# Optimization experiments

Hardware: AMD Instinct MI355X
Metric: run time of the kernel (lower is better)

## Reference

```python
import jax, jax.numpy as jnp
import numpy as np

LAMBDA_SCALE = 0.5
EPS = 1e-6

def setup_inputs() -> dict:
    key = jax.random.key(0)
    ks = jax.random.split(key, 9)
    B, S, D, E, F = 4, 2048, 1024, 8, 4096
    x = jax.random.normal(ks[0], (B, S, D), dtype=jnp.float32)
    prev_logits = jax.random.normal(ks[1], (B, S, E), dtype=jnp.float32)
    # router params (nn.Linear default init scale ~ 1/sqrt(fan_in))
    Wt = jax.random.normal(ks[2], (E, D), dtype=jnp.float32) / np.sqrt(D)
    Wgt = jax.random.normal(ks[3], (E, E), dtype=jnp.float32) / np.sqrt(E)
    We_logits = jnp.zeros((E,), dtype=jnp.float32)
    # expert MLPs, stacked over the expert axis
    W1 = jax.random.normal(ks[4], (E, D, F), dtype=jnp.float32) / np.sqrt(D)
    b1 = jax.random.normal(ks[5], (E, F), dtype=jnp.float32) * 0.01
    W2 = jax.random.normal(ks[6], (E, F, D), dtype=jnp.float32) / np.sqrt(F)
    b2 = jax.random.normal(ks[7], (E, D), dtype=jnp.float32) * 0.01
    return {"x": x, "prev_logits": prev_logits, "Wt": Wt, "Wgt": Wgt,
            "We_logits": We_logits, "W1": W1, "b1": b1, "W2": W2, "b2": b2}

def reference(x, prev_logits, Wt, Wgt, We_logits, W1, b1, W2, b2):
    # router logits: [B,S,E]
    logits = jnp.einsum('bsd,ed->bse', x, Wt) + jnp.einsum('bse,fe->bsf', prev_logits, Wgt)
    st = jax.nn.softmax(logits, axis=-1)
    We = jax.nn.sigmoid(We_logits)                      # [E]
    mask = (st > LAMBDA_SCALE * We).astype(st.dtype)    # data-dependent gate mask
    g = st * mask                                       # [B,S,E]
    # dense per-expert MLP over all tokens (faithful to the module)
    h = jax.nn.gelu(jnp.einsum('bsd,edf->bsef', x, W1) + b1, approximate=False)  # [B,S,E,F]
    outk = jnp.einsum('bsef,efd->bsed', h, W2) + b2     # [B,S,E,D]
    y = jnp.einsum('bse,bsed->bsd', g, outk)
    y = y / (jnp.sum(g, axis=-1, keepdims=True) + EPS)
    return (y, jax.lax.stop_gradient(logits))
```

## Files before the change

### kernel.cpp

```cpp
#include <hip/hip_runtime.h>
#include <math.h>

#define NTOK 8192
#define DDIM 1024
#define NEXP 8
#define FDIM 4096
#define MAXROWS 25600

typedef short bf16x8 __attribute__((ext_vector_type(8)));
typedef float f32x4 __attribute__((ext_vector_type(4)));

static __device__ __forceinline__ unsigned short f2bf(float f) {
  unsigned int u = __float_as_uint(f);
  u += 0x7fffu + ((u >> 16) & 1u);
  return (unsigned short)(u >> 16);
}

static __device__ __forceinline__ void gl_lds16(const void* g, void* l) {
  __builtin_amdgcn_global_load_lds(
      (const __attribute__((address_space(1))) unsigned int*)g,
      (__attribute__((address_space(3))) unsigned int*)l, 16, 0, 0);
}

__global__ __launch_bounds__(256) void router_kernel(
    const float* __restrict__ x, const float* __restrict__ prev,
    const float* __restrict__ Wt, const float* __restrict__ Wgt,
    const float* __restrict__ Wel,
    float* __restrict__ gn, float* __restrict__ logits_out)
{
  __shared__ float wt_s[NEXP * DDIM];
  const int tid = threadIdx.x;
  for (int i = tid; i < NEXP * DDIM; i += 256) wt_s[i] = Wt[i];
  __syncthreads();
  const int lane = tid & 63;
  const int t = blockIdx.x * 4 + (tid >> 6);

  const float* xr = x + (size_t)t * DDIM;
  float acc[NEXP];
#pragma unroll
  for (int e = 0; e < NEXP; ++e) acc[e] = 0.f;
  for (int k = lane; k < DDIM; k += 64) {
    float xv = xr[k];
#pragma unroll
    for (int e = 0; e < NEXP; ++e) acc[e] += xv * wt_s[e * DDIM + k];
  }
#pragma unroll
  for (int e = 0; e < NEXP; ++e) {
    float v = acc[e];
#pragma unroll
    for (int off = 32; off >= 1; off >>= 1) v += __shfl_xor(v, off);
    acc[e] = v;
  }
  float pl[NEXP];
#pragma unroll
  for (int e = 0; e < NEXP; ++e) pl[e] = prev[(size_t)t * NEXP + e];
#pragma unroll
  for (int e = 0; e < NEXP; ++e) {
    float s = acc[e];
#pragma unroll
    for (int e2 = 0; e2 < NEXP; ++e2) s += pl[e2] * Wgt[e * NEXP + e2];
    acc[e] = s;
  }
  float mx = acc[0];
#pragma unroll
  for (int e = 1; e < NEXP; ++e) mx = fmaxf(mx, acc[e]);
  float st[NEXP]; float se = 0.f;
#pragma unroll
  for (int e = 0; e < NEXP; ++e) { st[e] = expf(acc[e] - mx); se += st[e]; }
  float inv = 1.f / se;
  float g[NEXP]; float gs = 0.f;
#pragma unroll
  for (int e = 0; e < NEXP; ++e) {
    float s = st[e] * inv;
    float we = 1.f / (1.f + expf(-Wel[e]));
    float gg = (s > 0.5f * we) ? s : 0.f;
    g[e] = gg; gs += gg;
  }
  float r = 1.f / (gs + 1e-6f);
  if (lane < NEXP) {
    gn[(size_t)t * NEXP + lane] = g[lane] * r;
    logits_out[(size_t)t * NEXP + lane] = acc[lane];
  }
}

__global__ __launch_bounds__(256) void cast_kernel(
    const float* __restrict__ in, unsigned short* __restrict__ out)
{
  size_t i = ((size_t)blockIdx.x * 256 + threadIdx.x) * 8;
  float4 a = *(const float4*)(in + i);
  float4 b = *(const float4*)(in + i + 4);
  unsigned short tb[8];
  tb[0]=f2bf(a.x); tb[1]=f2bf(a.y); tb[2]=f2bf(a.z); tb[3]=f2bf(a.w);
  tb[4]=f2bf(b.x); tb[5]=f2bf(b.y); tb[6]=f2bf(b.z); tb[7]=f2bf(b.w);
  *(uint4*)(out + i) = *(const uint4*)tb;
}

__global__ __launch_bounds__(256) void count_kernel(
    const float* __restrict__ gn, int* __restrict__ cnt)
{
  const int e = blockIdx.x, tid = threadIdx.x;
  int c = 0;
  for (int t = tid; t < NTOK; t += 256) c += (gn[(size_t)t * NEXP + e] > 0.f) ? 1 : 0;
#pragma unroll
  for (int o = 32; o >= 1; o >>= 1) c += __shfl_xor(c, o);
  __shared__ int sm[4];
  if ((tid & 63) == 0) sm[tid >> 6] = c;
  __syncthreads();
  if (tid == 0) cnt[e] = sm[0] + sm[1] + sm[2] + sm[3];
}

__global__ __launch_bounds__(256) void compact_kernel(
    const float* __restrict__ gn, const int* __restrict__ cnt,
    int* __restrict__ offs, int* __restrict__ rowtok, int* __restrict__ rowof)
{
  const int e = blockIdx.x, tid = threadIdx.x;
  int base = 0;
#pragma unroll
  for (int q = 0; q < 8; ++q) if (q < e) base += (cnt[q] + 127) & ~127;
  const int padcnt = (cnt[e] + 127) & ~127;
  if (e == 0 && tid == 0) {
    int a = 0; offs[0] = 0;
#pragma unroll
    for (int q = 0; q < 8; ++q) { a += (cnt[q] + 127) & ~127; offs[q + 1] = a; }
  }
  __shared__ int wsm[4];
  __shared__ int running;
  if (tid == 0) running = 0;
  __syncthreads();
  const int lane = tid & 63, wv = tid >> 6;
  for (int c0 = 0; c0 < NTOK; c0 += 256) {
    const int t = c0 + tid;
    const bool pr = gn[(size_t)t * NEXP + e] > 0.f;
    unsigned long long bal = __ballot(pr);
    int pre = __popcll(bal & ((1ull << lane) - 1ull));
    if (lane == 0) wsm[wv] = __popcll(bal);
    __syncthreads();
    int wbase = 0;
#pragma unroll
    for (int q = 0; q < 4; ++q) if (q < wv) wbase += wsm[q];
    const int tot = wsm[0] + wsm[1] + wsm[2] + wsm[3];
    const int idx = base + running + wbase + pre;
    if (pr) rowtok[idx] = t;
    rowof[(size_t)t * NEXP + e] = pr ? idx : -1;
    __syncthreads();
    if (tid == 0) running += tot;
  }
  __syncthreads();
  for (int i = cnt[e] + tid; i < padcnt; i += 256) rowtok[base + i] = -1;
}

__global__ __launch_bounds__(256) void y_init_kernel(
    const float* __restrict__ gn, const float* __restrict__ b2,
    float* __restrict__ y)
{
  const int t = blockIdx.y;
  const int d = blockIdx.x * 256 + threadIdx.x;
  float s = 0.f;
#pragma unroll
  for (int e = 0; e < NEXP; ++e) s += gn[(size_t)t * NEXP + e] * b2[(size_t)e * DDIM + d];
  y[(size_t)t * DDIM + d] = s;
}

__global__ __launch_bounds__(256) void transcvt(
    const float* __restrict__ in, unsigned short* __restrict__ out,
    int Kin, int Nin)
{
  __shared__ float tile[64][65];
  const size_t zo = (size_t)blockIdx.z * Kin * Nin;
  const float* inp = in + zo;
  unsigned short* outp = out + zo;
  const int k0 = blockIdx.y * 64, n0 = blockIdx.x * 64;
  const int tid = threadIdx.x;
  const int r = tid >> 4, c4 = (tid & 15) * 4;
#pragma unroll
  for (int rr = 0; rr < 64; rr += 16) {
    float4 v = *(const float4*)(inp + (size_t)(k0 + r + rr) * Nin + n0 + c4);
    tile[r + rr][c4] = v.x; tile[r + rr][c4 + 1] = v.y;
    tile[r + rr][c4 + 2] = v.z; tile[r + rr][c4 + 3] = v.w;
  }
  __syncthreads();
#pragma unroll
  for (int it = 0; it < 2; ++it) {
    const int o = it * 256 + tid;
    const int n = o >> 3, ks = (o & 7) * 8;
    unsigned short tb[8];
#pragma unroll
    for (int j = 0; j < 8; ++j) tb[j] = f2bf(tile[ks + j][n]);
    *(uint4*)(outp + (size_t)(n0 + n) * Kin + k0 + ks) = *(const uint4*)tb;
  }
}

__global__ __launch_bounds__(256) void gemm_h(
    const unsigned short* __restrict__ xb,
    const unsigned short* __restrict__ W,
    size_t wstride,
    const float* __restrict__ b1,
    const float* __restrict__ gn,
    const int* __restrict__ rowtok,
    const int* __restrict__ offs,
    int efix,
    unsigned short* __restrict__ hb)
{
  __shared__ unsigned short As[128 * 32];
  __shared__ unsigned short Bs[128 * 32];
  __shared__ float gns[128];
  __shared__ float b1s[128];
  __shared__ int toks[128];
  const int tid = threadIdx.x;

  int mt, e, hbase;
  if (efix >= 0) {
    e = efix;
    hbase = offs[e];
    mt = (hbase >> 7) + blockIdx.y;
    if (mt * 128 >= offs[e + 1]) return;
  } else {
    mt = blockIdx.y;
    const int r0 = mt * 128;
    if (r0 >= offs[8]) return;
    e = 0;
#pragma unroll
    for (int q = 1; q < 8; ++q) if (r0 >= offs[q]) e = q;
    hbase = 0;
  }
  const int n0 = blockIdx.x * 128;
  const unsigned short* We = W + (size_t)e * wstride;

  if (tid < 128) {
    const int tk = rowtok[mt * 128 + tid];
    toks[tid] = tk;
    gns[tid] = (tk >= 0) ? gn[(size_t)tk * NEXP + e] : 0.f;
    b1s[tid] = b1[(size_t)e * FDIM + n0 + tid];
  }

  const int r0l = tid >> 2;
  const int cb = (tid & 3) * 8;
  int tka = rowtok[mt * 128 + r0l];      if (tka < 0) tka = 0;
  int tkb = rowtok[mt * 128 + 64 + r0l]; if (tkb < 0) tkb = 0;
  const unsigned short* ag0 = xb + (size_t)tka * DDIM + cb;
  const unsigned short* ag1 = xb + (size_t)tkb * DDIM + cb;
  const unsigned short* bg0 = We + (size_t)(n0 + r0l) * DDIM + cb;
  const unsigned short* bg1 = We + (size_t)(n0 + 64 + r0l) * DDIM + cb;
  const int w512 = (tid >> 6) * 512;
  unsigned short* la0 = As + w512;
  unsigned short* la1 = As + 2048 + w512;
  unsigned short* lb0 = Bs + w512;
  unsigned short* lb1 = Bs + 2048 + w512;

  const int lane = tid & 63;
  const int wm = ((tid >> 6) >> 1) * 64, wn = ((tid >> 6) & 1) * 64;
  const int fr = lane & 15, fk = (lane >> 4) * 8;

  f32x4 acc[4][4];
#pragma unroll
  for (int i = 0; i < 4; ++i)
#pragma unroll
    for (int j = 0; j < 4; ++j) acc[i][j] = (f32x4){0.f, 0.f, 0.f, 0.f};

  for (int k0 = 0; k0 < DDIM; k0 += 32) {
    __syncthreads();
    gl_lds16(ag0 + k0, la0);
    gl_lds16(ag1 + k0, la1);
    gl_lds16(bg0 + k0, lb0);
    gl_lds16(bg1 + k0, lb1);
    __syncthreads();
    bf16x8 af[4], bfv[4];
#pragma unroll
    for (int i = 0; i < 4; ++i) af[i] = *(const bf16x8*)&As[(wm + i * 16 + fr) * 32 + fk];
#pragma unroll
    for (int j = 0; j < 4; ++j) bfv[j] = *(const bf16x8*)&Bs[(wn + j * 16 + fr) * 32 + fk];
#pragma unroll
    for (int i = 0; i < 4; ++i)
#pragma unroll
      for (int j = 0; j < 4; ++j)
        acc[i][j] = __builtin_amdgcn_mfma_f32_16x16x32_bf16(af[i], bfv[j], acc[i][j], 0, 0, 0);
  }
#pragma unroll
  for (int i = 0; i < 4; ++i)
#pragma unroll
    for (int j = 0; j < 4; ++j) {
      const int col = wn + j * 16 + fr;
#pragma unroll
      for (int r = 0; r < 4; ++r) {
        const int row = wm + i * 16 + (lane >> 4) * 4 + r;
        if (toks[row] >= 0) {
          float v = acc[i][j][r] + b1s[col];
          v = 0.5f * v * (1.f + erff(v * 0.70710678118654752f));
          v *= gns[row];
          hb[(size_t)(mt * 128 + row - hbase) * FDIM + n0 + col] = f2bf(v);
        }
      }
    }
}

__global__ __launch_bounds__(256) void gemm_o(
    const unsigned short* __restrict__ hb,
    const unsigned short* __restrict__ W,
    size_t wstride,
    const int* __restrict__ rowtok,
    const int* __restrict__ offs,
    int efix,
    float* __restrict__ yout,
    int mode)
{
  __shared__ unsigned short As[128 * 32];
  __shared__ unsigned short Bs[128 * 32];
  __shared__ int toks[128];
  const int tid = threadIdx.x;

  int mt, e, hbase;
  if (efix >= 0) {
    e = efix;
    hbase = offs[e];
    mt = (hbase >> 7) + blockIdx.y;
    if (mt * 128 >= offs[e + 1]) return;
  } else {
    mt = blockIdx.y;
    const int r0 = mt * 128;
    if (r0 >= offs[8]) return;
    e = 0;
#pragma unroll
    for (int q = 1; q < 8; ++q) if (r0 >= offs[q]) e = q;
    hbase = 0;
  }
  const int n0 = blockIdx.x * 128;
  const unsigned short* We = W + (size_t)e * wstride;

  if (tid < 128) toks[tid] = rowtok[mt * 128 + tid];

  const int r0l = tid >> 2;
  const int cb = (tid & 3) * 8;
  const unsigned short* ag0 = hb + (size_t)(mt * 128 + r0l - hbase) * FDIM + cb;
  const unsigned short* ag1 = hb + (size_t)(mt * 128 + 64 + r0l - hbase) * FDIM + cb;
  const unsigned short* bg0 = We + (size_t)(n0 + r0l) * FDIM + cb;
  const unsigned short* bg1 = We + (size_t)(n0 + 64 + r0l) * FDIM + cb;
  const int w512 = (tid >> 6) * 512;
  unsigned short* la0 = As + w512;
  unsigned short* la1 = As + 2048 + w512;
  unsigned short* lb0 = Bs + w512;
  unsigned short* lb1 = Bs + 2048 + w512;

  const int lane = tid & 63;
  const int wm = ((tid >> 6) >> 1) * 64, wn = ((tid >> 6) & 1) * 64;
  const int fr = lane & 15, fk = (lane >> 4) * 8;

  f32x4 acc[4][4];
#pragma unroll
  for (int i = 0; i < 4; ++i)
#pragma unroll
    for (int j = 0; j < 4; ++j) acc[i][j] = (f32x4){0.f, 0.f, 0.f, 0.f};

  for (int k0 = 0; k0 < FDIM; k0 += 32) {
    __syncthreads();
    gl_lds16(ag0 + k0, la0);
    gl_lds16(ag1 + k0, la1);
    gl_lds16(bg0 + k0, lb0);
    gl_lds16(bg1 + k0, lb1);
    __syncthreads();
    bf16x8 af[4], bfv[4];
#pragma unroll
    for (int i = 0; i < 4; ++i) af[i] = *(const bf16x8*)&As[(wm + i * 16 + fr) * 32 + fk];
#pragma unroll
    for (int j = 0; j < 4; ++j) bfv[j] = *(const bf16x8*)&Bs[(wn + j * 16 + fr) * 32 + fk];
#pragma unroll
    for (int i = 0; i < 4; ++i)
#pragma unroll
      for (int j = 0; j < 4; ++j)
        acc[i][j] = __builtin_amdgcn_mfma_f32_16x16x32_bf16(af[i], bfv[j], acc[i][j], 0, 0, 0);
  }
#pragma unroll
  for (int i = 0; i < 4; ++i)
#pragma unroll
    for (int j = 0; j < 4; ++j) {
      const int col = wn + j * 16 + fr;
#pragma unroll
      for (int r = 0; r < 4; ++r) {
        const int row = wm + i * 16 + (lane >> 4) * 4 + r;
        if (mode == 0) {
          const int tk = toks[row];
          if (tk >= 0) yout[(size_t)tk * DDIM + n0 + col] += acc[i][j][r];
        } else {
          yout[(size_t)(mt * 128 + row) * DDIM + n0 + col] = acc[i][j][r];
        }
      }
    }
}

__global__ __launch_bounds__(256) void combine_kernel(
    const float* __restrict__ hb2, const int* __restrict__ rowof,
    const float* __restrict__ gn, const float* __restrict__ b2,
    float* __restrict__ y)
{
  const int t = blockIdx.y;
  const int d = blockIdx.x * 256 + threadIdx.x;
  float s = 0.f;
#pragma unroll
  for (int e = 0; e < NEXP; ++e) {
    s += gn[(size_t)t * NEXP + e] * b2[(size_t)e * DDIM + d];
    const int r = rowof[(size_t)t * NEXP + e];
    if (r >= 0) s += hb2[(size_t)r * DDIM + d];
  }
  y[(size_t)t * DDIM + d] = s;
}

extern "C" void kernel_launch(void* const* d_in, const int* in_sizes, int n_in,
                              void* d_out, int out_size, void* d_ws, size_t ws_size,
                              hipStream_t stream) {
  (void)in_sizes; (void)n_in; (void)out_size;
  const float* x    = (const float*)d_in[0];
  const float* prev = (const float*)d_in[1];
  const float* Wt   = (const float*)d_in[2];
  const float* Wgt  = (const float*)d_in[3];
  const float* Wel  = (const float*)d_in[4];
  const float* W1   = (const float*)d_in[5];
  const float* b1   = (const float*)d_in[6];
  const float* W2   = (const float*)d_in[7];
  const float* b2   = (const float*)d_in[8];

  float* y      = (float*)d_out;
  float* logits = y + (size_t)NTOK * DDIM;

  char* ws = (char*)d_ws;
  size_t pos = 0;
  auto take = [&](size_t bytes) -> char* {
    char* r = ws + pos; pos += (bytes + 255) & ~(size_t)255; return r;
  };
  float* gn            = (float*)take((size_t)NTOK * NEXP * 4);
  int* cnt             = (int*)take(64);
  int* offs            = (int*)take(64);
  int* rowtok          = (int*)take((size_t)MAXROWS * 4);
  int* rowof           = (int*)take((size_t)NTOK * NEXP * 4);
  unsigned short* xb   = (unsigned short*)take((size_t)NTOK * DDIM * 2);
  const size_t fixed = pos;

  const size_t wexp = (size_t)FDIM * DDIM;
  const size_t needA = fixed + 2 * NEXP * wexp * 2 + (size_t)MAXROWS * FDIM * 2
                       + (size_t)MAXROWS * DDIM * 4 + 4096;
  const bool tierA = ws_size >= needA;

  router_kernel<<<dim3(NTOK / 4), dim3(256), 0, stream>>>(x, prev, Wt, Wgt, Wel, gn, logits);
  cast_kernel<<<dim3((NTOK * DDIM) / (8 * 256)), dim3(256), 0, stream>>>(x, xb);
  count_kernel<<<dim3(NEXP), dim3(256), 0, stream>>>(gn, cnt);
  compact_kernel<<<dim3(NEXP), dim3(256), 0, stream>>>(gn, cnt, offs, rowtok, rowof);

  if (tierA) {
    unsigned short* W1b = (unsigned short*)take(NEXP * wexp * 2);
    unsigned short* W2b = (unsigned short*)take(NEXP * wexp * 2);
    unsigned short* hb  = (unsigned short*)take((size_t)MAXROWS * FDIM * 2);
    float* hb2          = (float*)take((size_t)MAXROWS * DDIM * 4);

    transcvt<<<dim3(FDIM / 64, DDIM / 64, NEXP), dim3(256), 0, stream>>>(W1, W1b, DDIM, FDIM);
    transcvt<<<dim3(DDIM / 64, FDIM / 64, NEXP), dim3(256), 0, stream>>>(W2, W2b, FDIM, DDIM);
    gemm_h<<<dim3(FDIM / 128, MAXROWS / 128), dim3(256), 0, stream>>>(
        xb, W1b, wexp, b1, gn, rowtok, offs, -1, hb);
    gemm_o<<<dim3(DDIM / 128, MAXROWS / 128), dim3(256), 0, stream>>>(
        hb, W2b, wexp, rowtok, offs, -1, hb2, 1);
    combine_kernel<<<dim3(DDIM / 256, NTOK), dim3(256), 0, stream>>>(hb2, rowof, gn, b2, y);
  } else {
    unsigned short* Wb = (unsigned short*)take(wexp * 2);
    unsigned short* hb = (unsigned short*)take((size_t)NTOK * FDIM * 2);

    y_init_kernel<<<dim3(DDIM / 256, NTOK), dim3(256), 0, stream>>>(gn, b2, y);
    for (int e = 0; e < NEXP; ++e) {
      transcvt<<<dim3(FDIM / 64, DDIM / 64, 1), dim3(256), 0, stream>>>(
          W1 + (size_t)e * wexp, Wb, DDIM, FDIM);
      gemm_h<<<dim3(FDIM / 128, 64), dim3(256), 0, stream>>>(
          xb, Wb, 0, b1, gn, rowtok, offs, e, hb);
      transcvt<<<dim3(DDIM / 64, FDIM / 64, 1), dim3(256), 0, stream>>>(
          W2 + (size_t)e * wexp, Wb, FDIM, DDIM);
      gemm_o<<<dim3(DDIM / 128, 64), dim3(256), 0, stream>>>(
          hb, Wb, 0, rowtok, offs, e, y, 0);
    }
  }
}
```

Before: 575.2 us.

## Double-buffer LDS tiles in expert GEMMs to overlap global loads with MFMA

Both expert GEMM kernels (gemm_h and gemm_o) now keep two LDS buffers for the A and B tiles. A prologue loads the first k-tile, and each iteration issues the async global-to-LDS loads for the next tile before running the MFMAs on the current one. This replaces two barriers per k-step with one, and hides global load latency behind compute. In exchange, LDS use per block doubles, which may lower occupancy. Correctness depends on the barrier waiting for the outstanding global_load_lds operations.

Result: faster. 524.5 us (-8.8%).

```diff
diff --git a/kernel.cpp b/kernel.cpp
--- a/kernel.cpp
+++ b/kernel.cpp
@@ -201,8 +201,8 @@
     int efix,
     unsigned short* __restrict__ hb)
 {
-  __shared__ unsigned short As[128 * 32];
-  __shared__ unsigned short Bs[128 * 32];
+  __shared__ unsigned short As[2][128 * 32];
+  __shared__ unsigned short Bs[2][128 * 32];
   __shared__ float gns[128];
   __shared__ float b1s[128];
   __shared__ int toks[128];
@@ -242,10 +242,10 @@
   const unsigned short* bg0 = We + (size_t)(n0 + r0l) * DDIM + cb;
   const unsigned short* bg1 = We + (size_t)(n0 + 64 + r0l) * DDIM + cb;
   const int w512 = (tid >> 6) * 512;
-  unsigned short* la0 = As + w512;
-  unsigned short* la1 = As + 2048 + w512;
-  unsigned short* lb0 = Bs + w512;
-  unsigned short* lb1 = Bs + 2048 + w512;
+  unsigned short* laA0 = &As[0][w512];
+  unsigned short* laA1 = &As[0][2048 + w512];
+  unsigned short* laB0 = &Bs[0][w512];
+  unsigned short* laB1 = &Bs[0][2048 + w512];
 
   const int lane = tid & 63;
   const int wm = ((tid >> 6) >> 1) * 64, wn = ((tid >> 6) & 1) * 64;
@@ -257,23 +257,33 @@
 #pragma unroll
     for (int j = 0; j < 4; ++j) acc[i][j] = (f32x4){0.f, 0.f, 0.f, 0.f};
 
+  gl_lds16(ag0, laA0); gl_lds16(ag1, laA1);
+  gl_lds16(bg0, laB0); gl_lds16(bg1, laB1);
+  __syncthreads();
+
+  int buf = 0;
   for (int k0 = 0; k0 < DDIM; k0 += 32) {
-    __syncthreads();
-    gl_lds16(ag0 + k0, la0);
-    gl_lds16(ag1 + k0, la1);
-    gl_lds16(bg0 + k0, lb0);
-    gl_lds16(bg1 + k0, lb1);
-    __syncthreads();
+    if (k0 + 32 < DDIM) {
+      const int o = (buf ^ 1) * 4096;
+      gl_lds16(ag0 + k0 + 32, laA0 + o);
+      gl_lds16(ag1 + k0 + 32, laA1 + o);
+      gl_lds16(bg0 + k0 + 32, laB0 + o);
+      gl_lds16(bg1 + k0 + 32, laB1 + o);
+    }
+    const unsigned short* Ab = &As[buf][0];
+    const unsigned short* Bb = &Bs[buf][0];
     bf16x8 af[4], bfv[4];
 #pragma unroll
-    for (int i = 0; i < 4; ++i) af[i] = *(const bf16x8*)&As[(wm + i * 16 + fr) * 32 + fk];
-#pragma unroll
-    for (int j = 0; j < 4; ++j) bfv[j] = *(const bf16x8*)&Bs[(wn + j * 16 + fr) * 32 + fk];
+    for (int i = 0; i < 4; ++i) af[i] = *(const bf16x8*)&Ab[(wm + i * 16 + fr) * 32 + fk];
+#pragma unroll
+    for (int j = 0; j < 4; ++j) bfv[j] = *(const bf16x8*)&Bb[(wn + j * 16 + fr) * 32 + fk];
 #pragma unroll
     for (int i = 0; i < 4; ++i)
 #pragma unroll
       for (int j = 0; j < 4; ++j)
         acc[i][j] = __builtin_amdgcn_mfma_f32_16x16x32_bf16(af[i], bfv[j], acc[i][j], 0, 0, 0);
+    __syncthreads();
+    buf ^= 1;
   }
 #pragma unroll
   for (int i = 0; i < 4; ++i)
@@ -303,8 +313,8 @@
     float* __restrict__ yout,
     int mode)
 {
-  __shared__ unsigned short As[128 * 32];
-  __shared__ unsigned short Bs[128 * 32];
+  __shared__ unsigned short As[2][128 * 32];
+  __shared__ unsigned short Bs[2][128 * 32];
   __shared__ int toks[128];
   const int tid = threadIdx.x;
 
@@ -335,10 +345,10 @@
   const unsigned short* bg0 = We + (size_t)(n0 + r0l) * FDIM + cb;
   const unsigned short* bg1 = We + (size_t)(n0 + 64 + r0l) * FDIM + cb;
   const int w512 = (tid >> 6) * 512;
-  unsigned short* la0 = As + w512;
-  unsigned short* la1 = As + 2048 + w512;
-  unsigned short* lb0 = Bs + w512;
-  unsigned short* lb1 = Bs + 2048 + w512;
+  unsigned short* laA0 = &As[0][w512];
+  unsigned short* laA1 = &As[0][2048 + w512];
+  unsigned short* laB0 = &Bs[0][w512];
+  unsigned short* laB1 = &Bs[0][2048 + w512];
 
   const int lane = tid & 63;
   const int wm = ((tid >> 6) >> 1) * 64, wn = ((tid >> 6) & 1) * 64;
@@ -350,23 +360,33 @@
 #pragma unroll
     for (int j = 0; j < 4; ++j) acc[i][j] = (f32x4){0.f, 0.f, 0.f, 0.f};
 
+  gl_lds16(ag0, laA0); gl_lds16(ag1, laA1);
+  gl_lds16(bg0, laB0); gl_lds16(bg1, laB1);
+  __syncthreads();
+
+  int buf = 0;
   for (int k0 = 0; k0 < FDIM; k0 += 32) {
-    __syncthreads();
-    gl_lds16(ag0 + k0, la0);
-    gl_lds16(ag1 + k0, la1);
-    gl_lds16(bg0 + k0, lb0);
-    gl_lds16(bg1 + k0, lb1);
-    __syncthreads();
+    if (k0 + 32 < FDIM) {
+      const int o = (buf ^ 1) * 4096;
+      gl_lds16(ag0 + k0 + 32, laA0 + o);
+      gl_lds16(ag1 + k0 + 32, laA1 + o);
+      gl_lds16(bg0 + k0 + 32, laB0 + o);
+      gl_lds16(bg1 + k0 + 32, laB1 + o);
+    }
+    const unsigned short* Ab = &As[buf][0];
+    const unsigned short* Bb = &Bs[buf][0];
     bf16x8 af[4], bfv[4];
 #pragma unroll
-    for (int i = 0; i < 4; ++i) af[i] = *(const bf16x8*)&As[(wm + i * 16 + fr) * 32 + fk];
-#pragma unroll
-    for (int j = 0; j < 4; ++j) bfv[j] = *(const bf16x8*)&Bs[(wn + j * 16 + fr) * 32 + fk];
+    for (int i = 0; i < 4; ++i) af[i] = *(const bf16x8*)&Ab[(wm + i * 16 + fr) * 32 + fk];
+#pragma unroll
+    for (int j = 0; j < 4; ++j) bfv[j] = *(const bf16x8*)&Bb[(wn + j * 16 + fr) * 32 + fk];
 #pragma unroll
     for (int i = 0; i < 4; ++i)
 #pragma unroll
       for (int j = 0; j < 4; ++j)
         acc[i][j] = __builtin_amdgcn_mfma_f32_16x16x32_bf16(af[i], bfv[j], acc[i][j], 0, 0, 0);
+    __syncthreads();
+    buf ^= 1;
   }
 #pragma unroll
   for (int i = 0; i < 4; ++i)
```

## Triple-buffer LDS tiles in expert GEMMs and use fast sigmoid-based GELU

Applied to the files above, without the earlier changes.

Both expert GEMM kernels now keep three LDS stages and prefetch two K-tiles ahead using direct global-to-LDS loads. Explicit vmcnt waits and barriers let global loads overlap MFMA compute instead of serializing load and compute each iteration. The exact erf GELU in the first GEMM's epilogue is replaced with an exp2/rcp sigmoid-style approximation, which cuts transcendental cost but changes numerics slightly. Tripling LDS use may lower occupancy.

Result: faster. 526.1 us (-8.5%).

```diff
diff --git a/kernel.cpp b/kernel.cpp
--- a/kernel.cpp
+++ b/kernel.cpp
@@ -10,6 +10,10 @@
 typedef short bf16x8 __attribute__((ext_vector_type(8)));
 typedef float f32x4 __attribute__((ext_vector_type(4)));
 
+#define BAR() asm volatile("s_barrier" ::: "memory")
+#define WAITV(n) asm volatile("s_waitcnt vmcnt(" #n ")" ::: "memory")
+#define WAITL() asm volatile("s_waitcnt lgkmcnt(0)" ::: "memory")
+
 static __device__ __forceinline__ unsigned short f2bf(float f) {
   unsigned int u = __float_as_uint(f);
   u += 0x7fffu + ((u >> 16) & 1u);
@@ -20,6 +24,13 @@
   __builtin_amdgcn_global_load_lds(
       (const __attribute__((address_space(1))) unsigned int*)g,
       (__attribute__((address_space(3))) unsigned int*)l, 16, 0, 0);
+}
+
+static __device__ __forceinline__ float gelu_f(float v) {
+  float x2 = v * v;
+  float p = fmaf(x2, 0.10294422f, 2.3021183f);
+  float E = __builtin_amdgcn_exp2f(v * p);
+  return v - v * __builtin_amdgcn_rcpf(E + 1.f);
 }
 
 __global__ __launch_bounds__(256) void router_kernel(
@@ -201,8 +212,8 @@
     int efix,
     unsigned short* __restrict__ hb)
 {
-  __shared__ unsigned short As[128 * 32];
-  __shared__ unsigned short Bs[128 * 32];
+  __shared__ unsigned short As[3][128 * 32];
+  __shared__ unsigned short Bs[3][128 * 32];
   __shared__ float gns[128];
   __shared__ float b1s[128];
   __shared__ int toks[128];
@@ -242,10 +253,8 @@
   const unsigned short* bg0 = We + (size_t)(n0 + r0l) * DDIM + cb;
   const unsigned short* bg1 = We + (size_t)(n0 + 64 + r0l) * DDIM + cb;
   const int w512 = (tid >> 6) * 512;
-  unsigned short* la0 = As + w512;
-  unsigned short* la1 = As + 2048 + w512;
-  unsigned short* lb0 = Bs + w512;
-  unsigned short* lb1 = Bs + 2048 + w512;
+  unsigned short* sA = &As[0][0];
+  unsigned short* sB = &Bs[0][0];
 
   const int lane = tid & 63;
   const int wm = ((tid >> 6) >> 1) * 64, wn = ((tid >> 6) & 1) * 64;
@@ -257,24 +266,41 @@
 #pragma unroll
     for (int j = 0; j < 4; ++j) acc[i][j] = (f32x4){0.f, 0.f, 0.f, 0.f};
 
-  for (int k0 = 0; k0 < DDIM; k0 += 32) {
-    __syncthreads();
-    gl_lds16(ag0 + k0, la0);
-    gl_lds16(ag1 + k0, la1);
-    gl_lds16(bg0 + k0, lb0);
-    gl_lds16(bg1 + k0, lb1);
-    __syncthreads();
+  auto stage = [&](int kt, int b) {
+    const int o = b * 4096;
+    gl_lds16(ag0 + kt * 32, sA + o + w512);
+    gl_lds16(ag1 + kt * 32, sA + o + 2048 + w512);
+    gl_lds16(bg0 + kt * 32, sB + o + w512);
+    gl_lds16(bg1 + kt * 32, sB + o + 2048 + w512);
+  };
+  auto compute = [&](int b) {
+    const unsigned short* Ab = sA + b * 4096;
+    const unsigned short* Bb = sB + b * 4096;
     bf16x8 af[4], bfv[4];
 #pragma unroll
-    for (int i = 0; i < 4; ++i) af[i] = *(const bf16x8*)&As[(wm + i * 16 + fr) * 32 + fk];
-#pragma unroll
-    for (int j = 0; j < 4; ++j) bfv[j] = *(const bf16x8*)&Bs[(wn + j * 16 + fr) * 32 + fk];
+    for (int i = 0; i < 4; ++i) af[i] = *(const bf16x8*)&Ab[(wm + i * 16 + fr) * 32 + fk];
+#pragma unroll
+    for (int j = 0; j < 4; ++j) bfv[j] = *(const bf16x8*)&Bb[(wn + j * 16 + fr) * 32 + fk];
 #pragma unroll
     for (int i = 0; i < 4; ++i)
 #pragma unroll
       for (int j = 0; j < 4; ++j)
         acc[i][j] = __builtin_amdgcn_mfma_f32_16x16x32_bf16(af[i], bfv[j], acc[i][j], 0, 0, 0);
-  }
+  };
+
+  const int NT = DDIM / 32;
+  stage(0, 0); stage(1, 1);
+  int t = 0;
+  for (; t + 2 < NT; ++t) {
+    stage(t + 2, (t + 2) % 3);
+    WAITV(8); BAR();
+    compute(t % 3);
+    WAITL(); __builtin_amdgcn_sched_barrier(0); BAR();
+  }
+  WAITV(0); BAR();
+  compute((NT - 2) % 3);
+  compute((NT - 1) % 3);
+
 #pragma unroll
   for (int i = 0; i < 4; ++i)
 #pragma unroll
@@ -284,9 +310,7 @@
       for (int r = 0; r < 4; ++r) {
         const int row = wm + i * 16 + (lane >> 4) * 4 + r;
         if (toks[row] >= 0) {
-          float v = acc[i][j][r] + b1s[col];
-          v = 0.5f * v * (1.f + erff(v * 0.70710678118654752f));
-          v *= gns[row];
+          float v = gelu_f(acc[i][j][r] + b1s[col]) * gns[row];
           hb[(size_t)(mt * 128 + row - hbase) * FDIM + n0 + col] = f2bf(v);
         }
       }
@@ -303,8 +327,8 @@
     float* __restrict__ yout,
     int mode)
 {
-  __shared__ unsigned short As[128 * 32];
-  __shared__ unsigned short Bs[128 * 32];
+  __shared__ unsigned short As[3][128 * 32];
+  __shared__ unsigned short Bs[3][128 * 32];
   __shared__ int toks[128];
   const int tid = threadIdx.x;
 
@@ -335,10 +359,8 @@
   const unsigned short* bg0 = We + (size_t)(n0 + r0l) * FDIM + cb;
   const unsigned short* bg1 = We + (size_t)(n0 + 64 + r0l) * FDIM + cb;
   const int w512 = (tid >> 6) * 512;
-  unsigned short* la0 = As + w512;
-  unsigned short* la1 = As + 2048 + w512;
-  unsigned short* lb0 = Bs + w512;
-  unsigned short* lb1 = Bs + 2048 + w512;
+  unsigned short* sA = &As[0][0];
+  unsigned short* sB = &Bs[0][0];
 
   const int lane = tid & 63;
   const int wm = ((tid >> 6) >> 1) * 64, wn = ((tid >> 6) & 1) * 64;
@@ -350,24 +372,41 @@
 #pragma unroll
     for (int j = 0; j < 4; ++j) acc[i][j] = (f32x4){0.f, 0.f, 0.f, 0.f};
 
-  for (int k0 = 0; k0 < FDIM; k0 += 32) {
-    __syncthreads();
-    gl_lds16(ag0 + k0, la0);
-    gl_lds16(ag1 + k0, la1);
-    gl_lds16(bg0 + k0, lb0);
-    gl_lds16(bg1 + k0, lb1);
-    __syncthreads();
+  auto stage = [&](int kt, int b) {
+    const int o = b * 4096;
+    gl_lds16(ag0 + kt * 32, sA + o + w512);
+    gl_lds16(ag1 + kt * 32, sA + o + 2048 + w512);
+    gl_lds16(bg0 + kt * 32, sB + o + w512);
+    gl_lds16(bg1 + kt * 32, sB + o + 2048 + w512);
+  };
+  auto compute = [&](int b) {
+    const unsigned short* Ab = sA + b * 4096;
+    const unsigned short* Bb = sB + b * 4096;
     bf16x8 af[4], bfv[4];
 #pragma unroll
-    for (int i = 0; i < 4; ++i) af[i] = *(const bf16x8*)&As[(wm + i * 16 + fr) * 32 + fk];
-#pragma unroll
-    for (int j = 0; j < 4; ++j) bfv[j] = *(const bf16x8*)&Bs[(wn + j * 16 + fr) * 32 + fk];
+    for (int i = 0; i < 4; ++i) af[i] = *(const bf16x8*)&Ab[(wm + i * 16 + fr) * 32 + fk];
+#pragma unroll
+    for (int j = 0; j < 4; ++j) bfv[j] = *(const bf16x8*)&Bb[(wn + j * 16 + fr) * 32 + fk];
 #pragma unroll
     for (int i = 0; i < 4; ++i)
 #pragma unroll
       for (int j = 0; j < 4; ++j)
         acc[i][j] = __builtin_amdgcn_mfma_f32_16x16x32_bf16(af[i], bfv[j], acc[i][j], 0, 0, 0);
-  }
+  };
+
+  const int NT = FDIM / 32;
+  stage(0, 0); stage(1, 1);
+  int t = 0;
+  for (; t + 2 < NT; ++t) {
+    stage(t + 2, (t + 2) % 3);
+    WAITV(8); BAR();
+    compute(t % 3);
+    WAITL(); __builtin_amdgcn_sched_barrier(0); BAR();
+  }
+  WAITV(0); BAR();
+  compute((NT - 2) % 3);
+  compute((NT - 1) % 3);
+
 #pragma unroll
   for (int i = 0; i < 4; ++i)
 #pragma unroll
```

## Double-buffer GEMM LDS tiles with swizzle, 2-wave blocks, fast GELU

Applied to the files above, without the earlier changes.

Both expert GEMMs now run 128-thread blocks of two waves, each wave computing a 128x64 tile. LDS holds two buffers, so the global-to-LDS load of the next K-slice is issued before the MFMAs on the current slice, with one wait plus barrier per step. An XOR swizzle on the LDS layout is meant to reduce bank conflicts. The exact erf GELU is replaced by a sigmoid-style exp2 approximation, which trades accuracy for fewer instructions. The larger accumulator array raises register pressure.

Result: faster. 546.4 us (-5.0%).

```diff
diff --git a/kernel.cpp b/kernel.cpp
--- a/kernel.cpp
+++ b/kernel.cpp
@@ -10,6 +10,9 @@
 typedef short bf16x8 __attribute__((ext_vector_type(8)));
 typedef float f32x4 __attribute__((ext_vector_type(4)));
 
+#define BAR() asm volatile("s_barrier" ::: "memory")
+#define WAITVL0() asm volatile("s_waitcnt vmcnt(0) lgkmcnt(0)" ::: "memory")
+
 static __device__ __forceinline__ unsigned short f2bf(float f) {
   unsigned int u = __float_as_uint(f);
   u += 0x7fffu + ((u >> 16) & 1u);
@@ -20,6 +23,13 @@
   __builtin_amdgcn_global_load_lds(
       (const __attribute__((address_space(1))) unsigned int*)g,
       (__attribute__((address_space(3))) unsigned int*)l, 16, 0, 0);
+}
+
+static __device__ __forceinline__ float gelu_f(float v) {
+  float x2 = v * v;
+  float p = fmaf(x2, 0.10294422f, 2.3021183f);
+  float E = __builtin_amdgcn_exp2f(v * p);
+  return v - v * __builtin_amdgcn_rcpf(E + 1.f);
 }
 
 __global__ __launch_bounds__(256) void router_kernel(
@@ -190,7 +200,8 @@
   }
 }
 
-__global__ __launch_bounds__(256) void gemm_h(
+
+__global__ __launch_bounds__(128, 2) void gemm_h(
     const unsigned short* __restrict__ xb,
     const unsigned short* __restrict__ W,
     size_t wstride,
@@ -201,8 +212,8 @@
     int efix,
     unsigned short* __restrict__ hb)
 {
-  __shared__ unsigned short As[128 * 32];
-  __shared__ unsigned short Bs[128 * 32];
+  __shared__ unsigned short As[2][4096];
+  __shared__ unsigned short Bs[2][4096];
   __shared__ float gns[128];
   __shared__ float b1s[128];
   __shared__ int toks[128];
@@ -226,74 +237,87 @@
   const int n0 = blockIdx.x * 128;
   const unsigned short* We = W + (size_t)e * wstride;
 
-  if (tid < 128) {
+  {
     const int tk = rowtok[mt * 128 + tid];
     toks[tid] = tk;
     gns[tid] = (tk >= 0) ? gn[(size_t)tk * NEXP + e] : 0.f;
     b1s[tid] = b1[(size_t)e * FDIM + n0 + tid];
   }
-
-  const int r0l = tid >> 2;
-  const int cb = (tid & 3) * 8;
-  int tka = rowtok[mt * 128 + r0l];      if (tka < 0) tka = 0;
-  int tkb = rowtok[mt * 128 + 64 + r0l]; if (tkb < 0) tkb = 0;
-  const unsigned short* ag0 = xb + (size_t)tka * DDIM + cb;
-  const unsigned short* ag1 = xb + (size_t)tkb * DDIM + cb;
-  const unsigned short* bg0 = We + (size_t)(n0 + r0l) * DDIM + cb;
-  const unsigned short* bg1 = We + (size_t)(n0 + 64 + r0l) * DDIM + cb;
-  const int w512 = (tid >> 6) * 512;
-  unsigned short* la0 = As + w512;
-  unsigned short* la1 = As + 2048 + w512;
-  unsigned short* lb0 = Bs + w512;
-  unsigned short* lb1 = Bs + 2048 + w512;
+  __syncthreads();
+
+  const int st_row = tid >> 2;
+  const int st_off = (((tid & 3) ^ (st_row & 3)) << 3);
+  const unsigned short* aP[4];
+  const unsigned short* bP[4];
+#pragma unroll
+  for (int i = 0; i < 4; ++i) {
+    int tk = toks[i * 32 + st_row]; if (tk < 0) tk = 0;
+    aP[i] = xb + (size_t)tk * DDIM + st_off;
+    bP[i] = We + (size_t)(n0 + i * 32 + st_row) * DDIM + st_off;
+  }
+  const int ldst = tid * 8;
 
   const int lane = tid & 63;
-  const int wm = ((tid >> 6) >> 1) * 64, wn = ((tid >> 6) & 1) * 64;
-  const int fr = lane & 15, fk = (lane >> 4) * 8;
-
-  f32x4 acc[4][4];
-#pragma unroll
-  for (int i = 0; i < 4; ++i)
+  const int w = tid >> 6;
+  const int fr = lane & 15;
+  const int rdoff = (((lane >> 4) ^ (lane & 3)) << 3);
+
+  f32x4 acc[8][4];
+#pragma unroll
+  for (int i = 0; i < 8; ++i)
 #pragma unroll
     for (int j = 0; j < 4; ++j) acc[i][j] = (f32x4){0.f, 0.f, 0.f, 0.f};
 
-  for (int k0 = 0; k0 < DDIM; k0 += 32) {
-    __syncthreads();
-    gl_lds16(ag0 + k0, la0);
-    gl_lds16(ag1 + k0, la1);
-    gl_lds16(bg0 + k0, lb0);
-    gl_lds16(bg1 + k0, lb1);
-    __syncthreads();
-    bf16x8 af[4], bfv[4];
-#pragma unroll
-    for (int i = 0; i < 4; ++i) af[i] = *(const bf16x8*)&As[(wm + i * 16 + fr) * 32 + fk];
-#pragma unroll
-    for (int j = 0; j < 4; ++j) bfv[j] = *(const bf16x8*)&Bs[(wn + j * 16 + fr) * 32 + fk];
-#pragma unroll
-    for (int i = 0; i < 4; ++i)
+  auto stage = [&](int kt, int b) {
+    const int ke = kt * 32;
+#pragma unroll
+    for (int i = 0; i < 4; ++i) {
+      gl_lds16(aP[i] + ke, &As[b][i * 1024 + ldst]);
+      gl_lds16(bP[i] + ke, &Bs[b][i * 1024 + ldst]);
+    }
+  };
+
+  const int NT = DDIM / 32;
+  stage(0, 0);
+  WAITVL0(); BAR();
+
+  for (int t = 0; t < NT; ++t) {
+    const int cur = t & 1;
+    if (t + 1 < NT) stage(t + 1, cur ^ 1);
+    bf16x8 af[8], bfv[4];
+#pragma unroll
+    for (int i = 0; i < 8; ++i)
+      af[i] = *(const bf16x8*)&As[cur][(i * 16 + fr) * 32 + rdoff];
+#pragma unroll
+    for (int j = 0; j < 4; ++j)
+      bfv[j] = *(const bf16x8*)&Bs[cur][(w * 64 + j * 16 + fr) * 32 + rdoff];
+#pragma unroll
+    for (int i = 0; i < 8; ++i)
 #pragma unroll
       for (int j = 0; j < 4; ++j)
         acc[i][j] = __builtin_amdgcn_mfma_f32_16x16x32_bf16(af[i], bfv[j], acc[i][j], 0, 0, 0);
-  }
-#pragma unroll
-  for (int i = 0; i < 4; ++i)
-#pragma unroll
-    for (int j = 0; j < 4; ++j) {
-      const int col = wn + j * 16 + fr;
-#pragma unroll
-      for (int r = 0; r < 4; ++r) {
-        const int row = wm + i * 16 + (lane >> 4) * 4 + r;
-        if (toks[row] >= 0) {
-          float v = acc[i][j][r] + b1s[col];
-          v = 0.5f * v * (1.f + erff(v * 0.70710678118654752f));
-          v *= gns[row];
-          hb[(size_t)(mt * 128 + row - hbase) * FDIM + n0 + col] = f2bf(v);
-        }
+    if (t + 1 < NT) { WAITVL0(); BAR(); }
+  }
+
+#pragma unroll
+  for (int i = 0; i < 8; ++i)
+#pragma unroll
+    for (int r = 0; r < 4; ++r) {
+      const int row = i * 16 + (lane >> 4) * 4 + r;
+      const int tk = toks[row];
+      if (tk < 0) continue;
+      const float gv = gns[row];
+      unsigned short* hrow = hb + (size_t)(mt * 128 + row - hbase) * FDIM + n0;
+#pragma unroll
+      for (int j = 0; j < 4; ++j) {
+        const int col = w * 64 + j * 16 + fr;
+        float v = gelu_f(acc[i][j][r] + b1s[col]) * gv;
+        hrow[col] = f2bf(v);
       }
     }
 }
 
-__global__ __launch_bounds__(256) void gemm_o(
+__global__ __launch_bounds__(128, 2) void gemm_o(
     const unsigned short* __restrict__ hb,
     const unsigned short* __restrict__ W,
     size_t wstride,
@@ -303,8 +327,8 @@
     float* __restrict__ yout,
     int mode)
 {
-  __shared__ unsigned short As[128 * 32];
-  __shared__ unsigned short Bs[128 * 32];
+  __shared__ unsigned short As[2][4096];
+  __shared__ unsigned short Bs[2][4096];
   __shared__ int toks[128];
   const int tid = threadIdx.x;
 
@@ -326,61 +350,82 @@
   const int n0 = blockIdx.x * 128;
   const unsigned short* We = W + (size_t)e * wstride;
 
-  if (tid < 128) toks[tid] = rowtok[mt * 128 + tid];
-
-  const int r0l = tid >> 2;
-  const int cb = (tid & 3) * 8;
-  const unsigned short* ag0 = hb + (size_t)(mt * 128 + r0l - hbase) * FDIM + cb;
-  const unsigned short* ag1 = hb + (size_t)(mt * 128 + 64 + r0l - hbase) * FDIM + cb;
-  const unsigned short* bg0 = We + (size_t)(n0 + r0l) * FDIM + cb;
-  const unsigned short* bg1 = We + (size_t)(n0 + 64 + r0l) * FDIM + cb;
-  const int w512 = (tid >> 6) * 512;
-  unsigned short* la0 = As + w512;
-  unsigned short* la1 = As + 2048 + w512;
-  unsigned short* lb0 = Bs + w512;
-  unsigned short* lb1 = Bs + 2048 + w512;
+  toks[tid] = rowtok[mt * 128 + tid];
+  __syncthreads();
+
+  const int st_row = tid >> 2;
+  const int st_off = (((tid & 3) ^ (st_row & 3)) << 3);
+  const unsigned short* aP[4];
+  const unsigned short* bP[4];
+#pragma unroll
+  for (int i = 0; i < 4; ++i) {
+    aP[i] = hb + (size_t)(mt * 128 - hbase + i * 32 + st_row) * FDIM + st_off;
+    bP[i] = We + (size_t)(n0 + i * 32 + st_row) * FDIM + st_off;
+  }
+  const int ldst = tid * 8;
 
   const int lane = tid & 63;
-  const int wm = ((tid >> 6) >> 1) * 64, wn = ((tid >> 6) & 1) * 64;
-  const int fr = lane & 15, fk = (lane >> 4) * 8;
-
-  f32x4 acc[4][4];
-#pragma unroll
-  for (int i = 0; i < 4; ++i)
+  const int w = tid >> 6;
+  const int fr = lane & 15;
+  const int rdoff = (((lane >> 4) ^ (lane & 3)) << 3);
+
+  f32x4 acc[8][4];
+#pragma unroll
+  for (int i = 0; i < 8; ++i)
 #pragma unroll
     for (int j = 0; j < 4; ++j) acc[i][j] = (f32x4){0.f, 0.f, 0.f, 0.f};
 
-  for (int k0 = 0; k0 < FDIM; k0 += 32) {
-    __syncthreads();
-    gl_lds16(ag0 + k0, la0);
-    gl_lds16(ag1 + k0, la1);
-    gl_lds16(bg0 + k0, lb0);
-    gl_lds16(bg1 + k0, lb1);
-    __syncthreads();
-    bf16x8 af[4], bfv[4];
-#pragma unroll
-    for (int i = 0; i < 4; ++i) af[i] = *(const bf16x8*)&As[(wm + i * 16 + fr) * 32 + fk];
-#pragma unroll
-    for (int j = 0; j < 4; ++j) bfv[j] = *(const bf16x8*)&Bs[(wn + j * 16 + fr) * 32 + fk];
-#pragma unroll
-    for (int i = 0; i < 4; ++i)
+  auto stage = [&](int kt, int b) {
+    const int ke = kt * 32;
+#pragma unroll
+    for (int i = 0; i < 4; ++i) {
+      gl_lds16(aP[i] + ke, &As[b][i * 1024 + ldst]);
+      gl_lds16(bP[i] + ke, &Bs[b][i * 1024 + ldst]);
+    }
+  };
+
+  const int NT = FDIM / 32;
+  stage(0, 0);
+  WAITVL0(); BAR();
+
+  for (int t = 0; t < NT; ++t) {
+    const int cur = t & 1;
+    if (t + 1 < NT) stage(t + 1, cur ^ 1);
+    bf16x8 af[8], bfv[4];
+#pragma unroll
+    for (int i = 0; i < 8; ++i)
+      af[i] = *(const bf16x8*)&As[cur][(i * 16 + fr) * 32 + rdoff];
+#pragma unroll
+    for (int j = 0; j < 4; ++j)
+      bfv[j] = *(const bf16x8*)&Bs[cur][(w * 64 + j * 16 + fr) * 32 + rdoff];
+#pragma unroll
+    for (int i = 0; i < 8; ++i)
 #pragma unroll
       for (int j = 0; j < 4; ++j)
         acc[i][j] = __builtin_amdgcn_mfma_f32_16x16x32_bf16(af[i], bfv[j], acc[i][j], 0, 0, 0);
-  }
-#pragma unroll
-  for (int i = 0; i < 4; ++i)
-#pragma unroll
-    for (int j = 0; j < 4; ++j) {
-      const int col = wn + j * 16 + fr;
-#pragma unroll
-      for (int r = 0; r < 4; ++r) {
-        const int row = wm + i * 16 + (lane >> 4) * 4 + r;
-        if (mode == 0) {
-          const int tk = toks[row];
-          if (tk >= 0) yout[(size_t)tk * DDIM + n0 + col] += acc[i][j][r];
-        } else {
-          yout[(size_t)(mt * 128 + row) * DDIM + n0 + col] = acc[i][j][r];
+    if (t + 1 < NT) { WAITVL0(); BAR(); }
+  }
+
+#pragma unroll
+  for (int i = 0; i < 8; ++i)
+#pragma unroll
+    for (int r = 0; r < 4; ++r) {
+      const int row = i * 16 + (lane >> 4) * 4 + r;
+      if (mode == 0) {
+        const int tk = toks[row];
+        if (tk < 0) continue;
+        float* yrow = yout + (size_t)tk * DDIM + n0;
+#pragma unroll
+        for (int j = 0; j < 4; ++j) {
+          const int col = w * 64 + j * 16 + fr;
+          yrow[col] += acc[i][j][r];
+        }
+      } else {
+        float* yrow = yout + (size_t)(mt * 128 + row) * DDIM + n0;
+#pragma unroll
+        for (int j = 0; j < 4; ++j) {
+          const int col = w * 64 + j * 16 + fr;
+          yrow[col] = acc[i][j][r];
         }
       }
     }
@@ -451,9 +496,9 @@
 
     transcvt<<<dim3(FDIM / 64, DDIM / 64, NEXP), dim3(256), 0, stream>>>(W1, W1b, DDIM, FDIM);
     transcvt<<<dim3(DDIM / 64, FDIM / 64, NEXP), dim3(256), 0, stream>>>(W2, W2b, FDIM, DDIM);
-    gemm_h<<<dim3(FDIM / 128, MAXROWS / 128), dim3(256), 0, stream>>>(
+    gemm_h<<<dim3(FDIM / 128, MAXROWS / 128), dim3(128), 0, stream>>>(
         xb, W1b, wexp, b1, gn, rowtok, offs, -1, hb);
-    gemm_o<<<dim3(DDIM / 128, MAXROWS / 128), dim3(256), 0, stream>>>(
+    gemm_o<<<dim3(DDIM / 128, MAXROWS / 128), dim3(128), 0, stream>>>(
         hb, W2b, wexp, rowtok, offs, -1, hb2, 1);
     combine_kernel<<<dim3(DDIM / 256, NTOK), dim3(256), 0, stream>>>(hb2, rowof, gn, b2, y);
   } else {
@@ -464,11 +509,11 @@
     for (int e = 0; e < NEXP; ++e) {
       transcvt<<<dim3(FDIM / 64, DDIM / 64, 1), dim3(256), 0, stream>>>(
           W1 + (size_t)e * wexp, Wb, DDIM, FDIM);
-      gemm_h<<<dim3(FDIM / 128, 64), dim3(256), 0, stream>>>(
+      gemm_h<<<dim3(FDIM / 128, 64), dim3(128), 0, stream>>>(
           xb, Wb, 0, b1, gn, rowtok, offs, e, hb);
       transcvt<<<dim3(DDIM / 64, FDIM / 64, 1), dim3(256), 0, stream>>>(
           W2 + (size_t)e * wexp, Wb, FDIM, DDIM);
-      gemm_o<<<dim3(DDIM / 128, 64), dim3(256), 0, stream>>>(
+      gemm_o<<<dim3(DDIM / 128, 64), dim3(128), 0, stream>>>(
           hb, Wb, 0, rowtok, offs, e, y, 0);
     }
   }
```
